# Optimization experiments

Hardware: AMD Instinct MI355X
Metric: run time of the kernel (lower is better)

The kernel has to match this reference:

```python
import jax, jax.numpy as jnp
import numpy as np

N_NODES = 50000


def gcn_conv(x, W, b, src, dst):
    # PyG GCNConv: h = x @ W; add self-loops; norm = deg^{-1/2}[src]*deg^{-1/2}[dst];
    # out = scatter_add(norm * h[src] -> dst) + bias
    h = x @ W  # [N, out]
    ones = jnp.ones(src.shape[0], dtype=x.dtype)
    deg = jax.ops.segment_sum(ones, dst, num_segments=N_NODES) + 1.0  # +1 for self-loop
    inv_sqrt = deg ** -0.5
    norm = inv_sqrt[src] * inv_sqrt[dst]  # [E]
    msgs = h[src] * norm[:, None]  # [E, out]
    agg = jax.ops.segment_sum(msgs, dst, num_segments=N_NODES)
    # self-loop contribution: norm_ii = deg_i^{-1}
    agg = agg + h * (inv_sqrt * inv_sqrt)[:, None]
    return agg + b


def setup_inputs() -> dict:
    key = jax.random.key(0)
    k1, k2, k3, k4 = jax.random.split(key, 4)
    d_in, d_h = 256, 256
    x = jax.random.normal(k1, (N_NODES, d_in), dtype=jnp.float32)
    edge_index = jax.random.randint(k2, (2, 800000), 0, N_NODES, dtype=jnp.int64)
    # Glorot-style params (GCNConv linear has no bias; separate bias added post-agg)
    W1 = jax.random.normal(k3, (d_in, d_h), dtype=jnp.float32) / np.sqrt(d_in)
    W2 = jax.random.normal(k4, (d_h, d_h), dtype=jnp.float32) / np.sqrt(d_h)
    b1 = jnp.zeros((d_h,), dtype=jnp.float32)
    b2 = jnp.zeros((d_h,), dtype=jnp.float32)
    return {"x": x, "edge_index": edge_index, "W1": W1, "b1": b1, "W2": W2, "b2": b2}


def reference(x, edge_index, W1, b1, W2, b2):
    src, dst = edge_index[0], edge_index[1]
    h = jax.nn.relu(gcn_conv(x, W1, b1, src, dst))
    h = jax.nn.relu(gcn_conv(h, W2, b2, src, dst))
    # global_mean_pool with batch=arange(N) assigns each node its own graph -> identity
    return h
```

## Files before the change

kernel.cpp:

```cpp
#include <hip/hip_runtime.h>
#include <hip/hip_bf16.h>

typedef unsigned short u16;
typedef unsigned int u32;

#define N_NODES 50000
#define N_EDGES 800000
#define DHID 256
#define NCHUNK 49

typedef __attribute__((ext_vector_type(8))) _Float16 f16x8;
typedef __attribute__((ext_vector_type(4))) float f32x4;
typedef __attribute__((ext_vector_type(2))) float f32x2;

__device__ __forceinline__ u16 f2bf(float f) {
    u32 u = __float_as_uint(f);
    u32 r = (u + 0x7FFFu + ((u >> 16) & 1u)) >> 16;
    return (u16)r;
}
__device__ __forceinline__ float bf2f(u32 bits16) {
    return __uint_as_float(bits16 << 16);
}
__device__ __forceinline__ u16 f2h(float f) {
    _Float16 h = (_Float16)f;
    union { _Float16 h; u16 u; } c; c.h = h;
    return c.u;
}
__device__ __forceinline__ void gl_lds16(const void* g, void* l) {
    __builtin_amdgcn_global_load_lds(
        (const __attribute__((address_space(1))) u32*)g,
        (__attribute__((address_space(3))) u32*)l, 16, 0, 0);
}

#define SPLIT_BLKS 12500
#define ZERO_BLKS 196
__global__ void prep_fused(const float* __restrict__ x, u16* __restrict__ xf,
                           const float* __restrict__ W1, const float* __restrict__ W2,
                           u16* __restrict__ W1t, u16* __restrict__ W2t,
                           int* __restrict__ deg, u32* __restrict__ hs32) {
    const int b = blockIdx.x, tid = threadIdx.x;
    if (b < SPLIT_BLKS) {
        int i = b * 256 + tid;
        float4 v = ((const float4*)x)[i];
        u16 h0 = f2h(v.x), h1 = f2h(v.y), h2 = f2h(v.z), h3 = f2h(v.w);
        uint2 hv;
        hv.x = (u32)h0 | ((u32)h1 << 16);
        hv.y = (u32)h2 | ((u32)h3 << 16);
        ((uint2*)xf)[i] = hv;
    } else if (b < SPLIT_BLKS + ZERO_BLKS) {
        int j = (b - SPLIT_BLKS) * 256 + tid;
        if (j < N_NODES) deg[j] = 0;
        if (j < 128) {
            int t = j >> 4, w = j & 15;
            hs32[((size_t)t * (N_NODES + 1) + N_NODES) * 16 + w] = 0;
        }
    } else {
        int idx = b - (SPLIT_BLKS + ZERO_BLKS);
        int y = idx >> 8, n = idx & 255, k = tid;
        const float* W = y ? W2 : W1;
        u16* o = y ? W2t : W1t;
        o[n * 256 + k] = f2h(W[k * 256 + n]);
    }
}

__global__ void deg_kernel(const int* __restrict__ dst, int* __restrict__ deg, int E) {
    int e = blockIdx.x * 256 + threadIdx.x;
    if (e < E) atomicAdd(&deg[dst[e]], 1);
}

__global__ __launch_bounds__(1024) void scan1_kernel(const int* __restrict__ deg,
                                                     int* __restrict__ partial,
                                                     int* __restrict__ totals, int n) {
    __shared__ int wsum[16];
    __shared__ int woff[16];
    const int tid = threadIdx.x, lane = tid & 63, wid = tid >> 6;
    const int idx = blockIdx.x * 1024 + tid;
    int v = (idx < n) ? deg[idx] : 0;
    int x = v;
#pragma unroll
    for (int off = 1; off < 64; off <<= 1) {
        int t = __shfl_up(x, off, 64);
        if (lane >= off) x += t;
    }
    if (lane == 63) wsum[wid] = x;
    __syncthreads();
    if (tid == 0) {
        int s = 0;
#pragma unroll
        for (int w = 0; w < 16; ++w) { woff[w] = s; s += wsum[w]; }
    }
    __syncthreads();
    x += woff[wid];
    partial[idx] = x;
    if (tid == 1023) totals[blockIdx.x] = x;
}

__global__ void scan3_kernel(const int* __restrict__ deg, const int* __restrict__ partial,
                             const int* __restrict__ totals, int* __restrict__ rptr,
                             int* __restrict__ cursor, int n) {
    __shared__ int coff_s;
    const int tid = threadIdx.x;
    const int mychunk = blockIdx.x >> 2;
    if (tid < 64) {
        int v = (tid < NCHUNK) ? totals[tid] : 0;
        int x = v;
#pragma unroll
        for (int off = 1; off < 64; off <<= 1) {
            int t = __shfl_up(x, off, 64);
            if (tid >= off) x += t;
        }
        if (tid == mychunk) coff_s = x - v;
    }
    __syncthreads();
    int i = blockIdx.x * 256 + tid;
    if (i < n) {
        int e = coff_s + partial[i] - deg[i];
        rptr[i] = e;
        cursor[i] = e;
    }
    if (i == 0) rptr[n] = N_EDGES;
}

__global__ void fill_kernel(const int* __restrict__ src, const int* __restrict__ dst,
                            int* __restrict__ cursor, u16* __restrict__ col16, int E) {
    int e = blockIdx.x * 256 + threadIdx.x;
    if (e < E) {
        int p = atomicAdd(&cursor[dst[e]], 1);
        col16[p] = (u16)src[e];
    }
}

__global__ __launch_bounds__(256) void gemm_f16_kernel(
    const u16* __restrict__ Af, const u16* __restrict__ Bt,
    const int* __restrict__ deg, u16* __restrict__ out, int M) {
    __shared__ u16 As[128 * 32];
    __shared__ u16 Bs[128 * 32];
    const int tid = threadIdx.x;
    const int wave = tid >> 6;
    const int lane = tid & 63;
    const int wm = wave >> 1, wn = wave & 1;
    const int quad = lane >> 4, l16 = lane & 15;
    const int m0 = blockIdx.x * 128;
    const int n0 = blockIdx.y * 128;

    f32x4 acc[4][4] = {};

    const int row0 = tid >> 2, row1 = (256 + tid) >> 2;
    const int kk = (tid & 3) * 8;
    int ar0 = m0 + row0; if (ar0 >= M) ar0 = M - 1;
    int ar1 = m0 + row1; if (ar1 >= M) ar1 = M - 1;
    const size_t aoff0 = (size_t)ar0 * 256 + kk;
    const size_t aoff1 = (size_t)ar1 * 256 + kk;
    const size_t boff0 = (size_t)(n0 + row0) * 256 + kk;
    const size_t boff1 = (size_t)(n0 + row1) * 256 + kk;
    const size_t l0 = (size_t)(wave * 64) * 8;
    const size_t l1 = (size_t)(256 + wave * 64) * 8;

    for (int ko = 0; ko < 8; ++ko) {
        const int koff = ko * 32;
        __syncthreads();
        gl_lds16(Af + aoff0 + koff, &As[l0]);
        gl_lds16(Af + aoff1 + koff, &As[l1]);
        gl_lds16(Bt + boff0 + koff, &Bs[l0]);
        gl_lds16(Bt + boff1 + koff, &Bs[l1]);
        asm volatile("s_waitcnt vmcnt(0)" ::: "memory");
        __syncthreads();

        f16x8 af[4], bf[4];
#pragma unroll
        for (int mi = 0; mi < 4; ++mi)
            af[mi] = *(const f16x8*)&As[(wm * 64 + mi * 16 + l16) * 32 + quad * 8];
#pragma unroll
        for (int ni = 0; ni < 4; ++ni)
            bf[ni] = *(const f16x8*)&Bs[(wn * 64 + ni * 16 + l16) * 32 + quad * 8];
#pragma unroll
        for (int mi = 0; mi < 4; ++mi)
#pragma unroll
            for (int ni = 0; ni < 4; ++ni)
                acc[mi][ni] = __builtin_amdgcn_mfma_f32_16x16x32_f16(af[mi], bf[ni], acc[mi][ni], 0, 0, 0);
    }

#pragma unroll
    for (int mi = 0; mi < 4; ++mi) {
#pragma unroll
        for (int r = 0; r < 4; ++r) {
            int row = m0 + wm * 64 + mi * 16 + quad * 4 + r;
            if (row < M) {
                float s = rsqrtf((float)deg[row] + 1.0f);
#pragma unroll
                for (int ni = 0; ni < 4; ++ni) {
                    int c = n0 + wn * 64 + ni * 16 + l16;
                    out[((size_t)(c >> 5) * (N_NODES + 1) + row) * 32 + (c & 31)] =
                        f2bf(acc[mi][ni][r] * s);
                }
            }
        }
    }
}

__global__ __launch_bounds__(256) void agg_kernel(
    const u16* __restrict__ hs, const int* __restrict__ rptr, const u16* __restrict__ col16,
    const float* __restrict__ bias,
    u16* __restrict__ out_f16, float* __restrict__ out_f,
    int mode, int Nn) {
    const int wave = threadIdx.x >> 6, lane = threadIdx.x & 63;
    const int t = blockIdx.x & 7;
    const int g = lane >> 3, ql = lane & 7;
    const int i = (blockIdx.x >> 3) * 32 + wave * 8 + g;
    const bool valid = (i < Nn);
    const int ii = valid ? i : (Nn - 1);
    const int beg = rptr[ii];
    const int cnt = rptr[ii + 1] - beg;
    int mc = cnt;
    mc = max(mc, __shfl_xor(mc, 8, 64));
    mc = max(mc, __shfl_xor(mc, 16, 64));
    mc = max(mc, __shfl_xor(mc, 32, 64));
    const u16* tbase = hs + (size_t)t * (N_NODES + 1) * 32;
    const int lq = ql * 4;

    f32x2 a01 = {0.f, 0.f}, a23 = {0.f, 0.f};
    const uint2 vself = *(const uint2*)(tbase + (size_t)ii * 32 + lq);

#define GIDX(j, e)                                                      \
    {                                                                   \
        int p = min((j), cnt - 1); p = max(p, 0);                       \
        int id = (int)col16[beg + p];                                   \
        e = ((j) < cnt) ? id : Nn;                                      \
    }
#define LOADP(e) (*(const uint2*)(tbase + (size_t)(e) * 32 + lq))
#define ACCUM(v)                                                        \
    {                                                                   \
        f32x2 p0, p1;                                                   \
        p0.x = __uint_as_float(v.x << 16);                              \
        p0.y = __uint_as_float(v.x & 0xffff0000u);                      \
        p1.x = __uint_as_float(v.y << 16);                              \
        p1.y = __uint_as_float(v.y & 0xffff0000u);                      \
        a01 += p0; a23 += p1;                                           \
    }

    if (mc > 0) {
        int e1;
        uint2 vA;
        { int e0; GIDX(0, e0); vA = LOADP(e0); }
        GIDX(1, e1);
        for (int j = 0; j < mc; ++j) {
            uint2 vB = {0, 0};
            int e2 = Nn;
            if (j + 1 < mc) {
                vB = LOADP(e1);
                GIDX(j + 2, e2);
            }
            ACCUM(vA);
            vA = vB; e1 = e2;
        }
    }
    ACCUM(vself);
#undef GIDX
#undef LOADP
#undef ACCUM

    const float inv = rsqrtf((float)cnt + 1.0f);
    const float4 bb = *(const float4*)(bias + t * 32 + lq);
    float r0 = fmaxf(fmaf(a01.x, inv, bb.x), 0.0f);
    float r1 = fmaxf(fmaf(a01.y, inv, bb.y), 0.0f);
    float r2 = fmaxf(fmaf(a23.x, inv, bb.z), 0.0f);
    float r3 = fmaxf(fmaf(a23.y, inv, bb.w), 0.0f);

    if (valid) {
        const size_t o = (size_t)i * 256 + t * 32 + lq;
        if (mode == 0) {
            u16 h0 = f2h(r0), h1 = f2h(r1), h2 = f2h(r2), h3 = f2h(r3);
            uint2 w;
            w.x = (u32)h0 | ((u32)h1 << 16);
            w.y = (u32)h2 | ((u32)h3 << 16);
            *(uint2*)(out_f16 + o) = w;
        } else {
            *(float4*)(out_f + o) = make_float4(r0, r1, r2, r3);
        }
    }
}

extern "C" void kernel_launch(void* const* d_in, const int* in_sizes, int n_in,
                              void* d_out, int out_size, void* d_ws, size_t ws_size,
                              hipStream_t stream) {
    const float* x = (const float*)d_in[0];
    const int* ei = (const int*)d_in[1];
    const float* W1 = (const float*)d_in[2];
    const float* b1 = (const float*)d_in[3];
    const float* W2 = (const float*)d_in[4];
    const float* b2 = (const float*)d_in[5];
    float* out = (float*)d_out;

    const int Nn = N_NODES, E = N_EDGES;
    const int* srcp = ei;
    const int* dstp = ei + E;

    u16* Af = (u16*)d_out;

    char* p = (char*)d_ws;
    auto take = [&](size_t bytes) -> void* {
        void* r = (void*)p;
        p += (bytes + 255) & ~(size_t)255;
        return r;
    };
    u16* hs      = (u16*)take((size_t)8 * (Nn + 1) * 32 * 2);
    u16* col16   = (u16*)take((size_t)E * 2);
    int* deg     = (int*)take((size_t)Nn * 4);
    int* cursor  = (int*)take((size_t)Nn * 4);
    int* rptr    = (int*)take((size_t)(Nn + 1) * 4);
    int* partial = (int*)take((size_t)NCHUNK * 1024 * 4);
    int* totals  = (int*)take(64 * 4);
    u16* W1t     = (u16*)take(256 * 256 * 2);
    u16* W2t     = (u16*)take(256 * 256 * 2);

    prep_fused<<<SPLIT_BLKS + ZERO_BLKS + 512, 256, 0, stream>>>(
        x, Af, W1, W2, W1t, W2t, deg, (u32*)hs);
    deg_kernel<<<E / 256, 256, 0, stream>>>(dstp, deg, E);
    scan1_kernel<<<NCHUNK, 1024, 0, stream>>>(deg, partial, totals, Nn);
    scan3_kernel<<<ZERO_BLKS, 256, 0, stream>>>(deg, partial, totals, rptr, cursor, Nn);
    fill_kernel<<<E / 256, 256, 0, stream>>>(srcp, dstp, cursor, col16, E);

    const int gm = (Nn + 127) / 128;
    const int aggblocks = ((Nn + 31) / 32) * 8;
    gemm_f16_kernel<<<dim3(gm, 2), 256, 0, stream>>>(Af, W1t, deg, hs, Nn);
    agg_kernel<<<aggblocks, 256, 0, stream>>>(hs, rptr, col16, b1, Af, nullptr, 0, Nn);
    gemm_f16_kernel<<<dim3(gm, 2), 256, 0, stream>>>(Af, W2t, deg, hs, Nn);
    agg_kernel<<<aggblocks, 256, 0, stream>>>(hs, rptr, col16, b2, nullptr, out, 1, Nn);
}
```

Baseline: 359.7 us.

## Sort nodes by degree, pad CSR rows to 4, widen aggregation loads

Adds a degree histogram, bin scan and scatter that build a degree-sorted node permutation, so the 16 nodes sharing a wave have similar edge counts and less divergence. CSR rows are padded to multiples of four with a sentinel index that points at a zero row. This lets the aggregation kernel fetch four neighbour indices at once and issue four 16-byte row loads per chunk. Each lane now covers 8 features instead of 4. The cost is three extra small launches, a padded column buffer to prefill, and scattered output writes caused by the permutation.

```diff
diff --git a/kernel.cpp b/kernel.cpp
--- a/kernel.cpp
+++ b/kernel.cpp
@@ -8,6 +8,7 @@
 #define N_EDGES 800000
 #define DHID 256
 #define NCHUNK 49
+#define PADCAP (1 << 20)
 
 typedef __attribute__((ext_vector_type(8))) _Float16 f16x8;
 typedef __attribute__((ext_vector_type(4))) float f32x4;
@@ -18,9 +19,6 @@
     u32 r = (u + 0x7FFFu + ((u >> 16) & 1u)) >> 16;
     return (u16)r;
 }
-__device__ __forceinline__ float bf2f(u32 bits16) {
-    return __uint_as_float(bits16 << 16);
-}
 __device__ __forceinline__ u16 f2h(float f) {
     _Float16 h = (_Float16)f;
     union { _Float16 h; u16 u; } c; c.h = h;
@@ -34,10 +32,13 @@
 
 #define SPLIT_BLKS 12500
 #define ZERO_BLKS 196
+#define W_BLKS 512
+#define PF_BLKS 512
 __global__ void prep_fused(const float* __restrict__ x, u16* __restrict__ xf,
                            const float* __restrict__ W1, const float* __restrict__ W2,
                            u16* __restrict__ W1t, u16* __restrict__ W2t,
-                           int* __restrict__ deg, u32* __restrict__ hs32) {
+                           int* __restrict__ deg, int* __restrict__ hist,
+                           u32* __restrict__ hs32, u16* __restrict__ col16p) {
     const int b = blockIdx.x, tid = threadIdx.x;
     if (b < SPLIT_BLKS) {
         int i = b * 256 + tid;
@@ -54,18 +55,48 @@
             int t = j >> 4, w = j & 15;
             hs32[((size_t)t * (N_NODES + 1) + N_NODES) * 16 + w] = 0;
         }
-    } else {
+        if (j < 64) hist[j] = 0;
+    } else if (b < SPLIT_BLKS + ZERO_BLKS + W_BLKS) {
         int idx = b - (SPLIT_BLKS + ZERO_BLKS);
         int y = idx >> 8, n = idx & 255, k = tid;
         const float* W = y ? W2 : W1;
         u16* o = y ? W2t : W1t;
         o[n * 256 + k] = f2h(W[k * 256 + n]);
+    } else {
+        int j = (b - (SPLIT_BLKS + ZERO_BLKS + W_BLKS)) * 256 + tid;
+        const u32 pat = (u32)N_NODES | ((u32)N_NODES << 16);
+        uint4 w; w.x = pat; w.y = pat; w.z = pat; w.w = pat;
+        ((uint4*)col16p)[j] = w;
     }
 }
 
 __global__ void deg_kernel(const int* __restrict__ dst, int* __restrict__ deg, int E) {
     int e = blockIdx.x * 256 + threadIdx.x;
     if (e < E) atomicAdd(&deg[dst[e]], 1);
+}
+
+__global__ void hist_kernel(const int* __restrict__ deg, int* __restrict__ hist, int n) {
+    int i = blockIdx.x * 256 + threadIdx.x;
+    if (i < n) atomicAdd(&hist[min(deg[i], 63)], 1);
+}
+__global__ void binscan_kernel(int* __restrict__ hist, int* __restrict__ bincur) {
+    const int l = threadIdx.x & 63;
+    int v = hist[l];
+    int x = v;
+#pragma unroll
+    for (int off = 1; off < 64; off <<= 1) {
+        int t = __shfl_up(x, off, 64);
+        if (l >= off) x += t;
+    }
+    bincur[l] = x - v;
+}
+__global__ void scatter_kernel(const int* __restrict__ deg, int* __restrict__ bincur,
+                               int* __restrict__ perm, int n) {
+    int i = blockIdx.x * 256 + threadIdx.x;
+    if (i < n) {
+        int pos = atomicAdd(&bincur[min(deg[i], 63)], 1);
+        perm[pos] = i;
+    }
 }
 
 __global__ __launch_bounds__(1024) void scan1_kernel(const int* __restrict__ deg,
@@ -75,7 +106,7 @@
     __shared__ int woff[16];
     const int tid = threadIdx.x, lane = tid & 63, wid = tid >> 6;
     const int idx = blockIdx.x * 1024 + tid;
-    int v = (idx < n) ? deg[idx] : 0;
+    int v = (idx < n) ? ((deg[idx] + 3) & ~3) : 0;
     int x = v;
 #pragma unroll
     for (int off = 1; off < 64; off <<= 1) {
@@ -96,7 +127,7 @@
 }
 
 __global__ void scan3_kernel(const int* __restrict__ deg, const int* __restrict__ partial,
-                             const int* __restrict__ totals, int* __restrict__ rptr,
+                             const int* __restrict__ totals, int* __restrict__ rp4,
                              int* __restrict__ cursor, int n) {
     __shared__ int coff_s;
     const int tid = threadIdx.x;
@@ -114,19 +145,19 @@
     __syncthreads();
     int i = blockIdx.x * 256 + tid;
     if (i < n) {
-        int e = coff_s + partial[i] - deg[i];
-        rptr[i] = e;
+        int pv = (deg[i] + 3) & ~3;
+        int e = coff_s + partial[i] - pv;
+        rp4[i] = e;
         cursor[i] = e;
     }
-    if (i == 0) rptr[n] = N_EDGES;
 }
 
 __global__ void fill_kernel(const int* __restrict__ src, const int* __restrict__ dst,
-                            int* __restrict__ cursor, u16* __restrict__ col16, int E) {
+                            int* __restrict__ cursor, u16* __restrict__ col16p, int E) {
     int e = blockIdx.x * 256 + threadIdx.x;
     if (e < E) {
         int p = atomicAdd(&cursor[dst[e]], 1);
-        col16[p] = (u16)src[e];
+        col16p[p] = (u16)src[e];
     }
 }
 
@@ -199,83 +230,93 @@
 }
 
 __global__ __launch_bounds__(256) void agg_kernel(
-    const u16* __restrict__ hs, const int* __restrict__ rptr, const u16* __restrict__ col16,
-    const float* __restrict__ bias,
-    u16* __restrict__ out_f16, float* __restrict__ out_f,
-    int mode, int Nn) {
+    const u16* __restrict__ hs, const int* __restrict__ rp4, const u16* __restrict__ col16p,
+    const int* __restrict__ deg, const int* __restrict__ perm, const float* __restrict__ bias,
+    u16* __restrict__ out_f16, float* __restrict__ out_f, int mode, int Nn) {
     const int wave = threadIdx.x >> 6, lane = threadIdx.x & 63;
     const int t = blockIdx.x & 7;
-    const int g = lane >> 3, ql = lane & 7;
-    const int i = (blockIdx.x >> 3) * 32 + wave * 8 + g;
-    const bool valid = (i < Nn);
-    const int ii = valid ? i : (Nn - 1);
-    const int beg = rptr[ii];
-    const int cnt = rptr[ii + 1] - beg;
-    int mc = cnt;
-    mc = max(mc, __shfl_xor(mc, 8, 64));
-    mc = max(mc, __shfl_xor(mc, 16, 64));
-    mc = max(mc, __shfl_xor(mc, 32, 64));
-    const u16* tbase = hs + (size_t)t * (N_NODES + 1) * 32;
-    const int lq = ql * 4;
-
-    f32x2 a01 = {0.f, 0.f}, a23 = {0.f, 0.f};
-    const uint2 vself = *(const uint2*)(tbase + (size_t)ii * 32 + lq);
-
-#define GIDX(j, e)                                                      \
-    {                                                                   \
-        int p = min((j), cnt - 1); p = max(p, 0);                       \
-        int id = (int)col16[beg + p];                                   \
-        e = ((j) < cnt) ? id : Nn;                                      \
-    }
-#define LOADP(e) (*(const uint2*)(tbase + (size_t)(e) * 32 + lq))
+    const int g = lane >> 2, ql = lane & 3;
+    const int k = (blockIdx.x >> 3) * 64 + wave * 16 + g;
+    const bool valid = (k < Nn);
+    const int i = perm[valid ? k : (Nn - 1)];
+    const int cnt = deg[i];
+    const int beg4 = rp4[i];
+    const int nch = (cnt + 3) >> 2;
+    int mch = nch;
+    mch = max(mch, __shfl_xor(mch, 4, 64));
+    mch = max(mch, __shfl_xor(mch, 8, 64));
+    mch = max(mch, __shfl_xor(mch, 16, 64));
+    mch = max(mch, __shfl_xor(mch, 32, 64));
+
+    const u16* tb = hs + (size_t)t * (N_NODES + 1) * 32;
+    const u32 lqo = (u32)ql * 8;
+    const uint4 vself = *(const uint4*)(tb + ((u32)i << 5) + lqo);
+
+    f32x2 a01 = {0.f, 0.f}, a23 = {0.f, 0.f}, a45 = {0.f, 0.f}, a67 = {0.f, 0.f};
+
+#define PLOAD(e) (*(const uint4*)(tb + ((u32)(e) << 5) + lqo))
+#define IADDR(c) (((c) < nch) ? (u32)(beg4 + (c) * 4) : (u32)(PADCAP - 4))
 #define ACCUM(v)                                                        \
     {                                                                   \
-        f32x2 p0, p1;                                                   \
-        p0.x = __uint_as_float(v.x << 16);                              \
-        p0.y = __uint_as_float(v.x & 0xffff0000u);                      \
-        p1.x = __uint_as_float(v.y << 16);                              \
-        p1.y = __uint_as_float(v.y & 0xffff0000u);                      \
-        a01 += p0; a23 += p1;                                           \
-    }
-
-    if (mc > 0) {
-        int e1;
-        uint2 vA;
-        { int e0; GIDX(0, e0); vA = LOADP(e0); }
-        GIDX(1, e1);
-        for (int j = 0; j < mc; ++j) {
-            uint2 vB = {0, 0};
-            int e2 = Nn;
-            if (j + 1 < mc) {
-                vB = LOADP(e1);
-                GIDX(j + 2, e2);
+        f32x2 q0, q1, q2, q3;                                           \
+        q0.x = __uint_as_float(v.x << 16);                              \
+        q0.y = __uint_as_float(v.x & 0xffff0000u);                      \
+        q1.x = __uint_as_float(v.y << 16);                              \
+        q1.y = __uint_as_float(v.y & 0xffff0000u);                      \
+        q2.x = __uint_as_float(v.z << 16);                              \
+        q2.y = __uint_as_float(v.z & 0xffff0000u);                      \
+        q3.x = __uint_as_float(v.w << 16);                              \
+        q3.y = __uint_as_float(v.w & 0xffff0000u);                      \
+        a01 += q0; a23 += q1; a45 += q2; a67 += q3;                     \
+    }
+
+    if (mch > 0) {
+        uint2 idc = *(const uint2*)(col16p + IADDR(0));
+        uint4 p0 = PLOAD(idc.x & 0xffffu), p1 = PLOAD(idc.x >> 16);
+        uint4 p2 = PLOAD(idc.y & 0xffffu), p3 = PLOAD(idc.y >> 16);
+        uint2 idn = *(const uint2*)(col16p + IADDR(1));
+#pragma unroll 2
+        for (int c = 0; c < mch; ++c) {
+            uint4 q0, q1, q2, q3;
+            const bool more = (c + 1 < mch);
+            if (more) {
+                q0 = PLOAD(idn.x & 0xffffu); q1 = PLOAD(idn.x >> 16);
+                q2 = PLOAD(idn.y & 0xffffu); q3 = PLOAD(idn.y >> 16);
+                idn = *(const uint2*)(col16p + IADDR(c + 2));
             }
-            ACCUM(vA);
-            vA = vB; e1 = e2;
+            ACCUM(p0); ACCUM(p1); ACCUM(p2); ACCUM(p3);
+            if (more) { p0 = q0; p1 = q1; p2 = q2; p3 = q3; }
         }
     }
     ACCUM(vself);
-#undef GIDX
-#undef LOADP
+#undef PLOAD
+#undef IADDR
 #undef ACCUM
 
     const float inv = rsqrtf((float)cnt + 1.0f);
-    const float4 bb = *(const float4*)(bias + t * 32 + lq);
-    float r0 = fmaxf(fmaf(a01.x, inv, bb.x), 0.0f);
-    float r1 = fmaxf(fmaf(a01.y, inv, bb.y), 0.0f);
-    float r2 = fmaxf(fmaf(a23.x, inv, bb.z), 0.0f);
-    float r3 = fmaxf(fmaf(a23.y, inv, bb.w), 0.0f);
+    const float4 b0 = *(const float4*)(bias + t * 32 + ql * 8);
+    const float4 b1 = *(const float4*)(bias + t * 32 + ql * 8 + 4);
+    float r0 = fmaxf(fmaf(a01.x, inv, b0.x), 0.0f);
+    float r1 = fmaxf(fmaf(a01.y, inv, b0.y), 0.0f);
+    float r2 = fmaxf(fmaf(a23.x, inv, b0.z), 0.0f);
+    float r3 = fmaxf(fmaf(a23.y, inv, b0.w), 0.0f);
+    float r4 = fmaxf(fmaf(a45.x, inv, b1.x), 0.0f);
+    float r5 = fmaxf(fmaf(a45.y, inv, b1.y), 0.0f);
+    float r6 = fmaxf(fmaf(a67.x, inv, b1.z), 0.0f);
+    float r7 = fmaxf(fmaf(a67.y, inv, b1.w), 0.0f);
 
     if (valid) {
-        const size_t o = (size_t)i * 256 + t * 32 + lq;
+        const size_t o = (size_t)i * 256 + t * 32 + ql * 8;
         if (mode == 0) {
-            u16 h0 = f2h(r0), h1 = f2h(r1), h2 = f2h(r2), h3 = f2h(r3);
-            uint2 w;
-            w.x = (u32)h0 | ((u32)h1 << 16);
-            w.y = (u32)h2 | ((u32)h3 << 16);
-            *(uint2*)(out_f16 + o) = w;
+            uint4 w;
+            w.x = (u32)f2h(r0) | ((u32)f2h(r1) << 16);
+            w.y = (u32)f2h(r2) | ((u32)f2h(r3) << 16);
+            w.z = (u32)f2h(r4) | ((u32)f2h(r5) << 16);
+            w.w = (u32)f2h(r6) | ((u32)f2h(r7) << 16);
+            *(uint4*)(out_f16 + o) = w;
         } else {
             *(float4*)(out_f + o) = make_float4(r0, r1, r2, r3);
+            *(float4*)(out_f + o + 4) = make_float4(r4, r5, r6, r7);
         }
     }
 }
@@ -304,26 +345,32 @@
         return r;
     };
     u16* hs      = (u16*)take((size_t)8 * (Nn + 1) * 32 * 2);
-    u16* col16   = (u16*)take((size_t)E * 2);
+    u16* col16p  = (u16*)take((size_t)PADCAP * 2);
     int* deg     = (int*)take((size_t)Nn * 4);
     int* cursor  = (int*)take((size_t)Nn * 4);
-    int* rptr    = (int*)take((size_t)(Nn + 1) * 4);
+    int* rp4     = (int*)take((size_t)Nn * 4);
     int* partial = (int*)take((size_t)NCHUNK * 1024 * 4);
     int* totals  = (int*)take(64 * 4);
+    int* hist    = (int*)take(64 * 4);
+    int* bincur  = (int*)take(64 * 4);
+    int* perm    = (int*)take((size_t)Nn * 4);
     u16* W1t     = (u16*)take(256 * 256 * 2);
     u16* W2t     = (u16*)take(256 * 256 * 2);
 
-    prep_fused<<<SPLIT_BLKS + ZERO_BLKS + 512, 256, 0, stream>>>(
-        x, Af, W1, W2, W1t, W2t, deg, (u32*)hs);
+    prep_fused<<<SPLIT_BLKS + ZERO_BLKS + W_BLKS + PF_BLKS, 256, 0, stream>>>(
+        x, Af, W1, W2, W1t, W2t, deg, hist, (u32*)hs, col16p);
     deg_kernel<<<E / 256, 256, 0, stream>>>(dstp, deg, E);
+    hist_kernel<<<ZERO_BLKS, 256, 0, stream>>>(deg, hist, Nn);
+    binscan_kernel<<<1, 64, 0, stream>>>(hist, bincur);
+    scatter_kernel<<<ZERO_BLKS, 256, 0, stream>>>(deg, bincur, perm, Nn);
     scan1_kernel<<<NCHUNK, 1024, 0, stream>>>(deg, partial, totals, Nn);
-    scan3_kernel<<<ZERO_BLKS, 256, 0, stream>>>(deg, partial, totals, rptr, cursor, Nn);
-    fill_kernel<<<E / 256, 256, 0, stream>>>(srcp, dstp, cursor, col16, E);
+    scan3_kernel<<<ZERO_BLKS, 256, 0, stream>>>(deg, partial, totals, rp4, cursor, Nn);
+    fill_kernel<<<E / 256, 256, 0, stream>>>(srcp, dstp, cursor, col16p, E);
 
     const int gm = (Nn + 127) / 128;
-    const int aggblocks = ((Nn + 31) / 32) * 8;
+    const int aggblocks = ((Nn + 63) / 64) * 8;
     gemm_f16_kernel<<<dim3(gm, 2), 256, 0, stream>>>(Af, W1t, deg, hs, Nn);
-    agg_kernel<<<aggblocks, 256, 0, stream>>>(hs, rptr, col16, b1, Af, nullptr, 0, Nn);
+    agg_kernel<<<aggblocks, 256, 0, stream>>>(hs, rp4, col16p, deg, perm, b1, Af, nullptr, 0, Nn);
     gemm_f16_kernel<<<dim3(gm, 2), 256, 0, stream>>>(Af, W2t, deg, hs, Nn);
-    agg_kernel<<<aggblocks, 256, 0, stream>>>(hs, rptr, col16, b2, nullptr, out, 1, Nn);
-}
+    agg_kernel<<<aggblocks, 256, 0, stream>>>(hs, rp4, col16p, deg, perm, b2, nullptr, out, 1, Nn);
+}
```

After: 608.4 us. 1.69x slower.
